# Optimization experiments

Measured on AMD Instinct MI355X. Metric: run time of the kernel, lower is better.

## Reference

```python
import jax, jax.numpy as jnp
import numpy as np

S = 512       # opt.resize_shape
DEPTH = 2     # opt.cattn_depth -> pooling window 2**DEPTH
P = 8         # opt.cattn_patch


def _interp_matrix(src, dst):
    # 1-D bilinear interpolation matrix, align_corners=True (matches F.interpolate)
    pos = jnp.linspace(0.0, src - 1.0, dst)
    lo = jnp.floor(pos).astype(jnp.int32)
    hi = jnp.minimum(lo + 1, src - 1)
    w = (pos - lo).astype(jnp.float32)
    idx = jnp.arange(dst)
    M = jnp.zeros((dst, src), jnp.float32)
    M = M.at[idx, lo].add(1.0 - w).at[idx, hi].add(w)
    return M


def setup_inputs() -> dict:
    key = jax.random.key(0)
    k1, k2, k3, k4 = jax.random.split(key, 4)
    x = jax.random.normal(k1, (4, 256, 64, 64), jnp.float32)
    attentions = jax.random.uniform(k2, (4, 8, 4096, 256), jnp.float32)
    conv_w = jax.random.normal(k3, (8, 256), jnp.float32) * 0.05
    conv_b = jax.random.normal(k4, (8,), jnp.float32) * 0.05
    return {"x": x, "attentions": attentions, "conv_w": conv_w, "conv_b": conv_b}


def reference(x, attentions, conv_w, conv_b):
    B, _, H, W = x.shape
    C = conv_w.shape[0]
    Kp = 2 ** DEPTH
    # 1x1 conv (ConvX)
    y = jnp.einsum('bchw,oc->bohw', x, conv_w) + conv_b[None, :, None, None]
    # bilinear upsample to (S, S), align_corners=True, separable matrices
    Mh, Mw = _interp_matrix(H, S), _interp_matrix(W, S)
    y = jnp.einsum('bchw,sh,tw->bcst', y, Mh, Mw)  # [B,C,S,S]
    # argmax one-hot (scatter of ones along class dim)
    am = jnp.argmax(y, axis=1)  # [B,S,S]
    onehot = (am[:, None] == jnp.arange(C)[None, :, None, None]).astype(y.dtype)
    # grouped conv of ones / Kp^2 == Kp x Kp mean pooling
    Sm = S // Kp
    fm = onehot.reshape(B, C, Sm, Kp, Sm, Kp).mean(axis=(3, 5))  # [B,C,Sm,Sm]
    # non-overlapping unfold PxP -> [B,C,P*P,L], torch Unfold ordering
    Lh = Sm // P
    unf = fm.reshape(B, C, Lh, P, Lh, P).transpose(0, 1, 3, 5, 2, 4).reshape(B, C, P * P, Lh * Lh)
    # per-class normalized attention matmul (vectorized over classes)
    nz = jnp.count_nonzero(attentions, axis=-1).astype(y.dtype)[..., None] + 1e-5  # [B,C,Q,1]
    corr = jnp.einsum('bcqk,bcpk->bcqp', attentions / nz, unf)  # [B,C,Q,P*P]
    # fold back to [B,C,S,S] (non-overlapping patches)
    Qh = S // P
    corr = corr.reshape(B, C, Qh, Qh, P, P).transpose(0, 1, 2, 4, 3, 5).reshape(B, C, S, S)
    out = jax.nn.log_softmax((corr + 1.0) * y, axis=1)
    return out, attentions
```

## Files before the change

### kernel.cpp

```cpp
#include <hip/hip_runtime.h>
#include <cstdint>

__global__ __launch_bounds__(256) void k_conv(const float* __restrict__ x,
                                              const float* __restrict__ w,
                                              const float* __restrict__ bias,
                                              float* __restrict__ y) {
  __shared__ float wl[2048];
  __shared__ float red[4][64][9];
  const int tid = threadIdx.x;
#pragma unroll
  for (int i = 0; i < 8; i++) { int idx = tid + i * 256; wl[idx] = w[idx]; }
  const int bi = blockIdx.x >> 6, row = blockIdx.x & 63;
  const int hwi = tid & 63, cg = tid >> 6;
  const float* xp = x + (((size_t)(bi * 256 + cg * 64)) * 64 + row) * 64 + hwi;
  float acc[8] = {0.f, 0.f, 0.f, 0.f, 0.f, 0.f, 0.f, 0.f};
  __syncthreads();
#pragma unroll 4
  for (int c = 0; c < 64; c++) {
    float v = xp[(size_t)c * 4096];
#pragma unroll
    for (int o = 0; o < 8; o++) acc[o] += v * wl[o * 256 + cg * 64 + c];
  }
#pragma unroll
  for (int o = 0; o < 8; o++) red[cg][hwi][o] = acc[o];
  __syncthreads();
#pragma unroll
  for (int i = 0; i < 2; i++) {
    int p = tid + i * 256; int o = p >> 6, hw = p & 63;
    float sv = red[0][hw][o] + red[1][hw][o] + red[2][hw][o] + red[3][hw][o] + bias[o];
    y[(((size_t)(bi * 8 + o)) * 64 + row) * 64 + hw] = sv;
  }
}

__global__ __launch_bounds__(256) void k_pool(const float* __restrict__ ys,
                                              float* __restrict__ fm) {
  const int g = blockIdx.x * 256 + threadIdx.x;
  const int bi = g >> 14, rem = g & 16383;
  const int sm = rem >> 7, tm = rem & 127;
  int cnt[8] = {0, 0, 0, 0, 0, 0, 0, 0};
  const float* yb = ys + (size_t)bi * 8 * 4096;
#pragma unroll
  for (int py = 0; py < 4; py++) {
    const int s = sm * 4 + py;
    float ph = s * (63.0f / 511.0f); int lh = (int)ph; float wh = ph - (float)lh;
    const int dh = (lh < 63) ? 64 : 0;
#pragma unroll
    for (int px = 0; px < 4; px++) {
      const int t = tm * 4 + px;
      float pw = t * (63.0f / 511.0f); int lt = (int)pw; float wt = pw - (float)lt;
      const int dt = (lt < 63) ? 1 : 0;
      const float w00 = (1.f - wh) * (1.f - wt), w01 = (1.f - wh) * wt;
      const float w10 = wh * (1.f - wt), w11 = wh * wt;
      const int base = lh * 64 + lt;
      float best = 0.f; int am = 0;
#pragma unroll
      for (int c = 0; c < 8; c++) {
        const float* yc = yb + c * 4096 + base;
        float v = w00 * yc[0] + w01 * yc[dt] + w10 * yc[dh] + w11 * yc[dh + dt];
        if (c == 0) { best = v; } else if (v > best) { best = v; am = c; }
      }
#pragma unroll
      for (int c = 0; c < 8; c++) cnt[c] += (am == c);
    }
  }
  const size_t ob = ((size_t)bi * 8) << 14;
#pragma unroll
  for (int c = 0; c < 8; c++)
    fm[ob + ((size_t)c << 14) + (sm << 7) + tm] = (float)cnt[c] * (1.0f / 16.0f);
}

__global__ __launch_bounds__(512, 4) void k_corr(const float* __restrict__ A,
                                                 const float* __restrict__ fm,
                                                 float* __restrict__ Aout,
                                                 float* __restrict__ corr,
                                                 float* __restrict__ nzinv) {
  __shared__ __align__(16) float At[32][260];
  __shared__ __align__(16) float Uts[32][64];
  __shared__ int nzc[256];
  const int tid = threadIdx.x;
  const int bc = blockIdx.y;
  const int qb = blockIdx.x << 8;
  const float* Ab = A + ((size_t)bc * 4096 + qb) * 256;
  float* Ob = Aout + ((size_t)bc * 4096 + qb) * 256;
  const float* fmb = fm + ((size_t)bc << 14);
  if (tid < 256) nzc[tid] = 0;
  const int lane = tid & 63, pg = tid >> 6, p0 = pg << 3;

  int fq[4], fk[4], ekk[4], ep[4];
#pragma unroll
  for (int i = 0; i < 4; i++) {
    const int f = tid + i * 512;
    fq[i] = f >> 3; fk[i] = (f & 7) * 4;
    ekk[i] = f >> 6; ep[i] = f & 63;
  }

  float4 ar[4]; float ur[4];
#pragma unroll
  for (int i = 0; i < 4; i++) ar[i] = *(const float4*)(Ab + (size_t)fq[i] * 256 + fk[i]);
#pragma unroll
  for (int i = 0; i < 4; i++) {
    const int l = ekk[i], p = ep[i];
    ur[i] = fmb[((l >> 4) * 8 + (p >> 3)) * 128 + (l & 15) * 8 + (p & 7)];
  }
  __syncthreads();
#pragma unroll
  for (int i = 0; i < 4; i++) {
    At[fk[i] + 0][fq[i]] = ar[i].x; At[fk[i] + 1][fq[i]] = ar[i].y;
    At[fk[i] + 2][fq[i]] = ar[i].z; At[fk[i] + 3][fq[i]] = ar[i].w;
    *(float4*)(Ob + (size_t)fq[i] * 256 + fk[i]) = ar[i];
    int c4 = (ar[i].x != 0.f) + (ar[i].y != 0.f) + (ar[i].z != 0.f) + (ar[i].w != 0.f);
    c4 += __shfl_xor(c4, 1); c4 += __shfl_xor(c4, 2); c4 += __shfl_xor(c4, 4);
    if ((tid & 7) == 0) atomicAdd(&nzc[fq[i]], c4);
    Uts[ekk[i]][ep[i]] = ur[i];
  }
  __syncthreads();

  float acc[4][8];
#pragma unroll
  for (int j = 0; j < 4; j++)
#pragma unroll
    for (int i = 0; i < 8; i++) acc[j][i] = 0.f;

  for (int c = 0; c < 8; c++) {
    if (c < 7) {
      const int kc = (c + 1) * 32;
#pragma unroll
      for (int i = 0; i < 4; i++) ar[i] = *(const float4*)(Ab + (size_t)fq[i] * 256 + kc + fk[i]);
#pragma unroll
      for (int i = 0; i < 4; i++) {
        const int l = kc + ekk[i], p = ep[i];
        ur[i] = fmb[((l >> 4) * 8 + (p >> 3)) * 128 + (l & 15) * 8 + (p & 7)];
      }
    }
#pragma unroll 8
    for (int kk = 0; kk < 32; kk++) {
      float4 a = *(const float4*)&At[kk][lane << 2];
      float4 u0 = *(const float4*)&Uts[kk][p0];
      float4 u1 = *(const float4*)&Uts[kk][p0 + 4];
      const float av[4] = {a.x, a.y, a.z, a.w};
      const float uv[8] = {u0.x, u0.y, u0.z, u0.w, u1.x, u1.y, u1.z, u1.w};
#pragma unroll
      for (int j = 0; j < 4; j++)
#pragma unroll
        for (int i = 0; i < 8; i++) acc[j][i] += av[j] * uv[i];
    }
    __syncthreads();
    if (c < 7) {
      const int kc = (c + 1) * 32;
#pragma unroll
      for (int i = 0; i < 4; i++) {
        At[fk[i] + 0][fq[i]] = ar[i].x; At[fk[i] + 1][fq[i]] = ar[i].y;
        At[fk[i] + 2][fq[i]] = ar[i].z; At[fk[i] + 3][fq[i]] = ar[i].w;
        *(float4*)(Ob + (size_t)fq[i] * 256 + kc + fk[i]) = ar[i];
        int c4 = (ar[i].x != 0.f) + (ar[i].y != 0.f) + (ar[i].z != 0.f) + (ar[i].w != 0.f);
        c4 += __shfl_xor(c4, 1); c4 += __shfl_xor(c4, 2); c4 += __shfl_xor(c4, 4);
        if ((tid & 7) == 0) atomicAdd(&nzc[fq[i]], c4);
        Uts[ekk[i]][ep[i]] = ur[i];
      }
    }
    __syncthreads();
  }

  if (tid < 256) nzinv[(size_t)bc * 4096 + qb + tid] = 1.0f / ((float)nzc[tid] + 1e-5f);

  float* cb = corr + (((size_t)bc * 4096 + qb + (lane << 2)) << 6) + p0;
#pragma unroll
  for (int j = 0; j < 4; j++) {
    float4 o0 = make_float4(acc[j][0], acc[j][1], acc[j][2], acc[j][3]);
    float4 o1 = make_float4(acc[j][4], acc[j][5], acc[j][6], acc[j][7]);
    *(float4*)(cb + ((size_t)j << 6)) = o0;
    *(float4*)(cb + ((size_t)j << 6) + 4) = o1;
  }
}

__global__ __launch_bounds__(256) void k_out(const float* __restrict__ corr,
                                             const float* __restrict__ nzinv,
                                             const float* __restrict__ ys,
                                             float* __restrict__ out) {
  const int g = blockIdx.x * 256 + threadIdx.x;
  const int b = g >> 18; const int s = (g >> 9) & 511; const int t = g & 511;
  const int q = ((s >> 3) << 6) + (t >> 3);
  const int p = ((s & 7) << 3) + (t & 7);
  float ph = s * (63.0f / 511.0f); int lh = (int)ph; float wh = ph - (float)lh;
  const int dh = (lh < 63) ? 64 : 0;
  float pw = t * (63.0f / 511.0f); int lt = (int)pw; float wt = pw - (float)lt;
  const int dt = (lt < 63) ? 1 : 0;
  const float w00 = (1.f - wh) * (1.f - wt), w01 = (1.f - wh) * wt;
  const float w10 = wh * (1.f - wt), w11 = wh * wt;
  const int base = lh * 64 + lt;
  float z[8];
#pragma unroll
  for (int c = 0; c < 8; c++) {
    const size_t bcp = (size_t)(b * 8 + c);
    const float cr = corr[(((bcp << 12) + q) << 6) + p];
    const float rz = nzinv[(bcp << 12) + q];
    const float* yc = ys + (bcp << 12) + base;
    const float yv = w00 * yc[0] + w01 * yc[dt] + w10 * yc[dh] + w11 * yc[dh + dt];
    z[c] = (cr * rz + 1.0f) * yv;
  }
  float m = z[0];
#pragma unroll
  for (int c = 1; c < 8; c++) m = fmaxf(m, z[c]);
  float sum = 0.f;
#pragma unroll
  for (int c = 0; c < 8; c++) sum += __expf(z[c] - m);
  const float ls = __logf(sum);
  const size_t ob = ((size_t)b << 21) + (s << 9) + t;
#pragma unroll
  for (int c = 0; c < 8; c++) out[ob + ((size_t)c << 18)] = z[c] - m - ls;
}

extern "C" void kernel_launch(void* const* d_in, const int* in_sizes, int n_in,
                              void* d_out, int out_size, void* d_ws, size_t ws_size,
                              hipStream_t stream) {
  const float* x   = (const float*)d_in[0];
  const float* att = (const float*)d_in[1];
  const float* cw  = (const float*)d_in[2];
  const float* cb  = (const float*)d_in[3];
  float* out1 = (float*)d_out;
  float* out2 = out1 + (size_t)4 * 8 * 512 * 512;
  float* ws = (float*)d_ws;
  float* y_small = ws;
  float* fm      = ws + 131072;
  float* nzinv   = ws + 655360;
  float* corr    = ws + 786432;

  k_conv<<<256, 256, 0, stream>>>(x, cw, cb, y_small);
  k_pool<<<256, 256, 0, stream>>>(y_small, fm);
  dim3 g4(16, 32);
  k_corr<<<g4, 512, 0, stream>>>(att, fm, out2, corr, nzinv);
  k_out<<<4096, 256, 0, stream>>>(corr, nzinv, y_small, out1);
}
```

Baseline: 327.2 us.

## Enlarge k_corr per-thread tile and stage row-interpolated logits in shared memory for k_out

```diff
diff --git a/kernel.cpp b/kernel.cpp
--- a/kernel.cpp
+++ b/kernel.cpp
@@ -69,7 +69,7 @@
     fm[ob + ((size_t)c << 14) + (sm << 7) + tm] = (float)cnt[c] * (1.0f / 16.0f);
 }
 
-__global__ __launch_bounds__(512, 4) void k_corr(const float* __restrict__ A,
+__global__ __launch_bounds__(256, 2) void k_corr(const float* __restrict__ A,
                                                  const float* __restrict__ fm,
                                                  float* __restrict__ Aout,
                                                  float* __restrict__ corr,
@@ -83,93 +83,93 @@
   const float* Ab = A + ((size_t)bc * 4096 + qb) * 256;
   float* Ob = Aout + ((size_t)bc * 4096 + qb) * 256;
   const float* fmb = fm + ((size_t)bc << 14);
-  if (tid < 256) nzc[tid] = 0;
-  const int lane = tid & 63, pg = tid >> 6, p0 = pg << 3;
-
-  int fq[4], fk[4], ekk[4], ep[4];
-#pragma unroll
-  for (int i = 0; i < 4; i++) {
-    const int f = tid + i * 512;
-    fq[i] = f >> 3; fk[i] = (f & 7) * 4;
-    ekk[i] = f >> 6; ep[i] = f & 63;
-  }
-
-  float4 ar[4]; float ur[4];
-#pragma unroll
-  for (int i = 0; i < 4; i++) ar[i] = *(const float4*)(Ab + (size_t)fq[i] * 256 + fk[i]);
-#pragma unroll
-  for (int i = 0; i < 4; i++) {
-    const int l = ekk[i], p = ep[i];
+  nzc[tid] = 0;
+  const int pg = tid & 7, qg = tid >> 3;
+  const int p0 = pg << 3, q0 = qg << 3;
+
+  int fq[8], fk[8], ul[8], up[8];
+#pragma unroll
+  for (int i = 0; i < 8; i++) {
+    const int f = tid + (i << 8);
+    fq[i] = f >> 3; fk[i] = (f & 7) << 2;
+    ul[i] = f >> 6; up[i] = f & 63;
+  }
+
+  float4 ar[8]; float ur[8];
+#pragma unroll
+  for (int i = 0; i < 8; i++) ar[i] = *(const float4*)(Ab + (size_t)fq[i] * 256 + fk[i]);
+#pragma unroll
+  for (int i = 0; i < 8; i++) {
+    const int l = ul[i], p = up[i];
     ur[i] = fmb[((l >> 4) * 8 + (p >> 3)) * 128 + (l & 15) * 8 + (p & 7)];
   }
   __syncthreads();
 #pragma unroll
-  for (int i = 0; i < 4; i++) {
+  for (int i = 0; i < 8; i++) {
     At[fk[i] + 0][fq[i]] = ar[i].x; At[fk[i] + 1][fq[i]] = ar[i].y;
     At[fk[i] + 2][fq[i]] = ar[i].z; At[fk[i] + 3][fq[i]] = ar[i].w;
     *(float4*)(Ob + (size_t)fq[i] * 256 + fk[i]) = ar[i];
     int c4 = (ar[i].x != 0.f) + (ar[i].y != 0.f) + (ar[i].z != 0.f) + (ar[i].w != 0.f);
     c4 += __shfl_xor(c4, 1); c4 += __shfl_xor(c4, 2); c4 += __shfl_xor(c4, 4);
     if ((tid & 7) == 0) atomicAdd(&nzc[fq[i]], c4);
-    Uts[ekk[i]][ep[i]] = ur[i];
-  }
-  __syncthreads();
-
-  float acc[4][8];
-#pragma unroll
-  for (int j = 0; j < 4; j++)
+    Uts[ul[i]][up[i]] = ur[i];
+  }
+  __syncthreads();
+
+  float acc[8][8];
+#pragma unroll
+  for (int j = 0; j < 8; j++)
 #pragma unroll
     for (int i = 0; i < 8; i++) acc[j][i] = 0.f;
 
   for (int c = 0; c < 8; c++) {
     if (c < 7) {
-      const int kc = (c + 1) * 32;
-#pragma unroll
-      for (int i = 0; i < 4; i++) ar[i] = *(const float4*)(Ab + (size_t)fq[i] * 256 + kc + fk[i]);
-#pragma unroll
-      for (int i = 0; i < 4; i++) {
-        const int l = kc + ekk[i], p = ep[i];
+      const int kc = (c + 1) << 5;
+#pragma unroll
+      for (int i = 0; i < 8; i++) ar[i] = *(const float4*)(Ab + (size_t)fq[i] * 256 + kc + fk[i]);
+#pragma unroll
+      for (int i = 0; i < 8; i++) {
+        const int l = kc + ul[i], p = up[i];
         ur[i] = fmb[((l >> 4) * 8 + (p >> 3)) * 128 + (l & 15) * 8 + (p & 7)];
       }
     }
 #pragma unroll 8
     for (int kk = 0; kk < 32; kk++) {
-      float4 a = *(const float4*)&At[kk][lane << 2];
+      float4 a0 = *(const float4*)&At[kk][q0];
+      float4 a1 = *(const float4*)&At[kk][q0 + 4];
       float4 u0 = *(const float4*)&Uts[kk][p0];
       float4 u1 = *(const float4*)&Uts[kk][p0 + 4];
-      const float av[4] = {a.x, a.y, a.z, a.w};
+      const float av[8] = {a0.x, a0.y, a0.z, a0.w, a1.x, a1.y, a1.z, a1.w};
       const float uv[8] = {u0.x, u0.y, u0.z, u0.w, u1.x, u1.y, u1.z, u1.w};
 #pragma unroll
-      for (int j = 0; j < 4; j++)
+      for (int j = 0; j < 8; j++)
 #pragma unroll
         for (int i = 0; i < 8; i++) acc[j][i] += av[j] * uv[i];
     }
     __syncthreads();
     if (c < 7) {
-      const int kc = (c + 1) * 32;
-#pragma unroll
-      for (int i = 0; i < 4; i++) {
+      const int kc = (c + 1) << 5;
+#pragma unroll
+      for (int i = 0; i < 8; i++) {
         At[fk[i] + 0][fq[i]] = ar[i].x; At[fk[i] + 1][fq[i]] = ar[i].y;
         At[fk[i] + 2][fq[i]] = ar[i].z; At[fk[i] + 3][fq[i]] = ar[i].w;
         *(float4*)(Ob + (size_t)fq[i] * 256 + kc + fk[i]) = ar[i];
         int c4 = (ar[i].x != 0.f) + (ar[i].y != 0.f) + (ar[i].z != 0.f) + (ar[i].w != 0.f);
         c4 += __shfl_xor(c4, 1); c4 += __shfl_xor(c4, 2); c4 += __shfl_xor(c4, 4);
         if ((tid & 7) == 0) atomicAdd(&nzc[fq[i]], c4);
-        Uts[ekk[i]][ep[i]] = ur[i];
+        Uts[ul[i]][up[i]] = ur[i];
       }
     }
     __syncthreads();
   }
 
-  if (tid < 256) nzinv[(size_t)bc * 4096 + qb + tid] = 1.0f / ((float)nzc[tid] + 1e-5f);
-
-  float* cb = corr + (((size_t)bc * 4096 + qb + (lane << 2)) << 6) + p0;
-#pragma unroll
-  for (int j = 0; j < 4; j++) {
-    float4 o0 = make_float4(acc[j][0], acc[j][1], acc[j][2], acc[j][3]);
-    float4 o1 = make_float4(acc[j][4], acc[j][5], acc[j][6], acc[j][7]);
-    *(float4*)(cb + ((size_t)j << 6)) = o0;
-    *(float4*)(cb + ((size_t)j << 6) + 4) = o1;
+  nzinv[(size_t)bc * 4096 + qb + tid] = 1.0f / ((float)nzc[tid] + 1e-5f);
+
+#pragma unroll
+  for (int j = 0; j < 8; j++) {
+    float* cb = corr + (((size_t)bc * 4096 + qb + q0 + j) << 6) + p0;
+    *(float4*)cb       = make_float4(acc[j][0], acc[j][1], acc[j][2], acc[j][3]);
+    *(float4*)(cb + 4) = make_float4(acc[j][4], acc[j][5], acc[j][6], acc[j][7]);
   }
 }
 
@@ -177,37 +177,63 @@
                                              const float* __restrict__ nzinv,
                                              const float* __restrict__ ys,
                                              float* __restrict__ out) {
-  const int g = blockIdx.x * 256 + threadIdx.x;
-  const int b = g >> 18; const int s = (g >> 9) & 511; const int t = g & 511;
-  const int q = ((s >> 3) << 6) + (t >> 3);
-  const int p = ((s & 7) << 3) + (t & 7);
-  float ph = s * (63.0f / 511.0f); int lh = (int)ph; float wh = ph - (float)lh;
-  const int dh = (lh < 63) ? 64 : 0;
-  float pw = t * (63.0f / 511.0f); int lt = (int)pw; float wt = pw - (float)lt;
-  const int dt = (lt < 63) ? 1 : 0;
-  const float w00 = (1.f - wh) * (1.f - wt), w01 = (1.f - wh) * wt;
-  const float w10 = wh * (1.f - wt), w11 = wh * wt;
-  const int base = lh * 64 + lt;
-  float z[8];
+  __shared__ float G[2][8][65];
+  const int bx = blockIdx.x;
+  const int b = bx >> 8;
+  const int s0 = (bx & 255) << 1;
+  const int tid = threadIdx.x;
+  const float* ysb = ys + ((size_t)b << 15);
+#pragma unroll
+  for (int j = 0; j < 4; j++) {
+    const int e = tid + (j << 8);
+    const int sl = e >> 9, c = (e >> 6) & 7, l = e & 63;
+    const int s = s0 + sl;
+    float ph = s * (63.0f / 511.0f); int lh = (int)ph; float wh = ph - (float)lh;
+    const int dh = (lh < 63) ? 64 : 0;
+    const float* yc = ysb + ((size_t)c << 12) + lh * 64 + l;
+    G[sl][c][l] = (1.f - wh) * yc[0] + wh * yc[dh];
+  }
+  __syncthreads();
+
+  const int sl = tid >> 7;
+  const int s = s0 + sl;
+  const int t0 = (tid & 127) << 2;
+  const int q = ((s >> 3) << 6) + (t0 >> 3);
+  const int p0 = ((s & 7) << 3) + (t0 & 7);
+
+  float z[4][8];
 #pragma unroll
   for (int c = 0; c < 8; c++) {
     const size_t bcp = (size_t)(b * 8 + c);
-    const float cr = corr[(((bcp << 12) + q) << 6) + p];
+    const float4 cr = *(const float4*)&corr[(((bcp << 12) + q) << 6) + p0];
     const float rz = nzinv[(bcp << 12) + q];
-    const float* yc = ys + (bcp << 12) + base;
-    const float yv = w00 * yc[0] + w01 * yc[dt] + w10 * yc[dh] + w11 * yc[dh + dt];
-    z[c] = (cr * rz + 1.0f) * yv;
-  }
-  float m = z[0];
-#pragma unroll
-  for (int c = 1; c < 8; c++) m = fmaxf(m, z[c]);
-  float sum = 0.f;
-#pragma unroll
-  for (int c = 0; c < 8; c++) sum += __expf(z[c] - m);
-  const float ls = __logf(sum);
-  const size_t ob = ((size_t)b << 21) + (s << 9) + t;
-#pragma unroll
-  for (int c = 0; c < 8; c++) out[ob + ((size_t)c << 18)] = z[c] - m - ls;
+    const float crv[4] = {cr.x, cr.y, cr.z, cr.w};
+#pragma unroll
+    for (int u = 0; u < 4; u++) {
+      const float pw = (t0 + u) * (63.0f / 511.0f);
+      const int lt = (int)pw; const float wtt = pw - (float)lt;
+      const int hi = (lt < 63) ? lt + 1 : 63;
+      const float yv = (1.f - wtt) * G[sl][c][lt] + wtt * G[sl][c][hi];
+      z[u][c] = (crv[u] * rz + 1.0f) * yv;
+    }
+  }
+  const size_t ob = ((size_t)b << 21) + ((size_t)s << 9) + t0;
+#pragma unroll
+  for (int c = 0; c < 8; c++) {
+    float4 o;
+#pragma unroll
+    for (int u = 0; u < 4; u++) {
+      float m = z[u][0];
+#pragma unroll
+      for (int cc = 1; cc < 8; cc++) m = fmaxf(m, z[u][cc]);
+      float sum = 0.f;
+#pragma unroll
+      for (int cc = 0; cc < 8; cc++) sum += __expf(z[u][cc] - m);
+      const float v = z[u][c] - m - __logf(sum);
+      if (u == 0) o.x = v; else if (u == 1) o.y = v; else if (u == 2) o.z = v; else o.w = v;
+    }
+    *(float4*)&out[ob + ((size_t)c << 18)] = o;
+  }
 }
 
 extern "C" void kernel_launch(void* const* d_in, const int* in_sizes, int n_in,
@@ -228,6 +254,6 @@
   k_conv<<<256, 256, 0, stream>>>(x, cw, cb, y_small);
   k_pool<<<256, 256, 0, stream>>>(y_small, fm);
   dim3 g4(16, 32);
-  k_corr<<<g4, 512, 0, stream>>>(att, fm, out2, corr, nzinv);
-  k_out<<<4096, 256, 0, stream>>>(corr, nzinv, y_small, out1);
-}
+  k_corr<<<g4, 256, 0, stream>>>(att, fm, out2, corr, nzinv);
+  k_out<<<1024, 256, 0, stream>>>(corr, nzinv, y_small, out1);
+}
```

After: 332.7 us. Within noise of the previous version (+1.7%).
